# Performance work log

Hardware: AMD Instinct MI355X
Metric: run time of the kernel (lower is better)

The kernel has to match this reference:

```python
import jax, jax.numpy as jnp
from jax import lax
import numpy as np

SCALES = [1.0, 0.9, 0.8, 0.7, 0.6]
SOFTMAX_SCALE = 10.0
RES_SCALE = 1.0
EPS = 1e-4  # escape_NaN buffer


def prelu(x, a):
    # torch nn.PReLU with a single shared parameter a
    return jnp.where(x >= 0, x, a * x)


def conv1x1(x, W, b):
    # x: [B,Cin,H,W], W: [Cout,Cin], b: [Cout]
    return jnp.einsum('oi,bihw->bohw', W, x) + b[None, :, None, None]


def extract_patches(x):
    # x: [B,C,H,W] -> [B, H*W, C, 3, 3]; 'same' padding (pad 1), stride 1,
    # matching F.unfold channel ordering (C, kh, kw) and row-major spatial order.
    B, C, H, W = x.shape
    p = jnp.pad(x, ((0, 0), (0, 0), (1, 1), (1, 1)))
    shifts = [p[:, :, i:i + H, j:j + W] for i in range(3) for j in range(3)]
    pat = jnp.stack(shifts, axis=-1)                      # [B,C,H,W,9]
    pat = pat.reshape(B, C, H, W, 3, 3)
    return pat.transpose(0, 2, 3, 1, 4, 5).reshape(B, H * W, C, 3, 3)


def setup_inputs() -> dict:
    key = jax.random.key(0)
    ks = jax.random.split(key, 7)
    B, C, H, W = 4, 64, 48, 48
    red = 2
    x = jax.random.normal(ks[0], (B, C, H, W), jnp.float32)
    # conv_match_L_base: 1x1 conv 64->32 + PReLU
    Wb = jax.random.normal(ks[1], (C // red, C), jnp.float32) * 0.05
    bb = jax.random.normal(ks[2], (C // red,), jnp.float32) * 0.05
    ab = jnp.asarray(0.25, jnp.float32)
    # conv_match: 1x1 conv 64->32 + PReLU
    Wm = jax.random.normal(ks[3], (C // red, C), jnp.float32) * 0.05
    bm = jax.random.normal(ks[4], (C // red,), jnp.float32) * 0.05
    am = jnp.asarray(0.25, jnp.float32)
    # conv_assembly: 1x1 conv 64->64 + PReLU
    Wa = jax.random.normal(ks[5], (C, C), jnp.float32) * 0.05
    ba = jax.random.normal(ks[6], (C,), jnp.float32) * 0.05
    aa = jnp.asarray(0.25, jnp.float32)
    return {"x": x, "Wb": Wb, "bb": bb, "ab": ab,
            "Wm": Wm, "bm": bm, "am": am,
            "Wa": Wa, "ba": ba, "aa": aa}


def reference(x, Wb, bb, ab, Wm, bm, am, Wa, ba, aa):
    B, C, H, W = x.shape
    match_base = prelu(conv1x1(x, Wb, bb), ab)  # [B,32,H,W]

    w_list, raw_list = [], []
    for s in SCALES:
        if s != 1.0:
            Hs, Ws = int(H * s), int(W * s)
            ref = jax.image.resize(x, (B, C, Hs, Ws), 'bilinear', antialias=False)
        else:
            ref = x
        base = prelu(conv1x1(ref, Wa, ba), aa)   # [B,64,Hs,Ws]
        mat = prelu(conv1x1(ref, Wm, bm), am)    # [B,32,Hs,Ws]
        raw_list.append(extract_patches(base))   # [B,Ls,64,3,3]
        w_list.append(extract_patches(mat))      # [B,Ls,32,3,3]

    wall = jnp.concatenate(w_list, axis=1)       # [B,N,32,3,3]
    rawall = jnp.concatenate(raw_list, axis=1)   # [B,N,64,3,3]
    norm = jnp.maximum(jnp.sqrt(jnp.sum(wall * wall, axis=(2, 3, 4), keepdims=True)), EPS)
    wn = wall / norm

    dn = ('NCHW', 'OIHW', 'NCHW')

    def per_sample(xb, wb, rb):
        # xb: [32,H,W], wb: [N,32,3,3], rb: [N,64,3,3]
        scores = lax.conv_general_dilated(xb[None], wb, (1, 1), ((1, 1), (1, 1)),
                                          dimension_numbers=dn)       # [1,N,H,W]
        attn = jax.nn.softmax(scores * SOFTMAX_SCALE, axis=1)
        # conv_transpose2d(attn, rb, stride=1, padding=1) == conv with flipped,
        # channel-swapped kernel and padding 1
        kt = jnp.flip(rb, axis=(2, 3)).transpose(1, 0, 2, 3)           # [64,N,3,3]
        out = lax.conv_general_dilated(attn, kt, (1, 1), ((1, 1), (1, 1)),
                                       dimension_numbers=dn)           # [1,64,H,W]
        return out[0] / 4.0

    y = jax.vmap(per_sample)(match_base, wn, rawall)  # [B,64,H,W]
    return y + x * RES_SCALE
```

## Files before the change

kernel.cpp:

```cpp
#include <hip/hip_runtime.h>
#include <hip/hip_bf16.h>
#include <hip/hip_fp16.h>

typedef __half h16;
typedef _Float16 f16;
typedef f16 f16x8 __attribute__((ext_vector_type(8)));
typedef __attribute__((ext_vector_type(4))) float f32x4;

#define NB 4
#define NCH 64
#define HW 2304
#define NP 7470
#define NPAD 7552
#define NT 236
#define NT2 118
#define NBLK 59
#define SW2 NPAD

__device__ __forceinline__ float us2f(unsigned short u){
  unsigned v = (unsigned)u << 16; float f; __builtin_memcpy(&f, &v, 4); return f;
}
__device__ __forceinline__ void gl16(const void* g, void* l){
  __builtin_amdgcn_global_load_lds((const __attribute__((address_space(1))) unsigned int*)g,
                                   (__attribute__((address_space(3))) unsigned int*)l, 16, 0, 0);
}

__device__ __forceinline__ void n_decode(int n, int& off, int& d, int& y, int& x){
  if (n < 2304)      { off = 0;    d = 48; }
  else if (n < 4153) { off = 2304; d = 43; }
  else if (n < 5597) { off = 4153; d = 38; }
  else if (n < 6686) { off = 5597; d = 33; }
  else               { off = 6686; d = 28; }
  int l = n - off; y = l / d; x = l - y * d;
}

__global__ __launch_bounds__(256) void k_detect(const void* __restrict__ x, int* __restrict__ flag){
  const unsigned short* u = (const unsigned short*)x;
  int tid = threadIdx.x;
  int c = 0;
  for (int i = tid; i < 8192; i += 256){
    float v = us2f(u[i]);
    float a = fabsf(v);
    if (v == 0.f || (a > 1e-5f && a < 1e3f)) c++;
  }
  #pragma unroll
  for (int o = 1; o < 64; o <<= 1) c += __shfl_xor(c, o);
  __shared__ int wr[4];
  if ((tid & 63) == 0) wr[tid >> 6] = c;
  __syncthreads();
  if (tid == 0) flag[0] = ((wr[0]+wr[1]+wr[2]+wr[3]) > 7000) ? 1 : 0;
}

struct CanonArgs { const void* src[10]; float* dst[10]; int end[10]; };

__global__ __launch_bounds__(256) void k_canon_all(CanonArgs a, int tot, const int* __restrict__ flag){
  int id = blockIdx.x * 256 + threadIdx.x;
  if (id >= tot) return;
  int k = 0;
  while (id >= a.end[k]) k++;
  int local = id - (k ? a.end[k-1] : 0);
  float v;
  if (flag[0]) v = us2f(((const unsigned short*)a.src[k])[local]);
  else         v = ((const float*)a.src[k])[local];
  a.dst[k][local] = v;
}

__global__ __launch_bounds__(256) void k_resize(const float* __restrict__ x, h16* __restrict__ xs){
  int id = blockIdx.x * 256 + threadIdx.x;
  if (id >= NB * NCH * NP) return;
  int b = id / (NCH*NP), rem = id - b*(NCH*NP);
  int c = rem / NP, n = rem - c*NP;
  int off, d, y, xx; n_decode(n, off, d, y, xx);
  const float* pc = x + ((size_t)b * NCH + c) * HW;
  float v;
  if (off == 0){
    v = pc[y*48 + xx];
  } else {
    float cy = (y + 0.5f) * (48.0f / (float)d) - 0.5f;
    float cx = (xx + 0.5f) * (48.0f / (float)d) - 0.5f;
    int y0 = (int)floorf(cy), x0 = (int)floorf(cx);
    float fy = cy - (float)y0, fx = cx - (float)x0;
    int y1 = min(y0 + 1, 47), x1 = min(x0 + 1, 47);
    y0 = max(y0, 0); x0 = max(x0, 0);
    v = (1.f-fy)*((1.f-fx)*pc[y0*48+x0] + fx*pc[y0*48+x1])
      + fy*((1.f-fx)*pc[y1*48+x0] + fx*pc[y1*48+x1]);
  }
  xs[id] = __float2half(v);
}

template<bool OB>
__global__ __launch_bounds__(256) void k_conv1x1(const h16* __restrict__ in, const float* __restrict__ Wt,
    const float* __restrict__ bias, const float* __restrict__ alpha, void* __restrict__ outv,
    int npix, int cout, size_t in_bstride, size_t out_bstride, int rs_in, int rs_out){
  __shared__ float Wl[64*64];
  __shared__ float it[64][64];
  int b = blockIdx.y;
  int n0 = blockIdx.x * 64;
  int tid = threadIdx.x;
  const h16* ib = in + (size_t)b * in_bstride;
  for (int i = tid; i < cout * 64; i += 256) Wl[i] = Wt[i];
  for (int i = tid; i < 64 * 64; i += 256){
    int ci = i >> 6, nn = i & 63;
    int n = n0 + nn;
    it[ci][nn] = (n < npix) ? __half2float(ib[(size_t)ci * rs_in + n]) : 0.f;
  }
  __syncthreads();
  float al = alpha[0];
  for (int oi = tid; oi < cout * 64; oi += 256){
    int co = oi >> 6, nn = oi & 63;
    float acc = bias[co];
    #pragma unroll
    for (int ci = 0; ci < 64; ci++) acc = fmaf(Wl[co*64+ci], it[ci][nn], acc);
    acc = acc >= 0.f ? acc : al * acc;
    int n = n0 + nn;
    if (n < npix){
      size_t idx = (size_t)b * out_bstride + (size_t)co * rs_out + n;
      if constexpr (OB) ((h16*)outv)[idx] = __float2half(acc);
      else              ((float*)outv)[idx] = acc;
    }
  }
}

__global__ __launch_bounds__(256) void k_sq(const float* __restrict__ mat, float* __restrict__ q){
  int id = blockIdx.x * 256 + threadIdx.x;
  if (id >= NB * NP) return;
  int b = id / NP, n = id - b * NP;
  const float* mp = mat + (size_t)b * 32 * NP + n;
  float s = 0.f;
  #pragma unroll
  for (int c = 0; c < 32; c++){ float v = mp[(size_t)c * NP]; s += v * v; }
  q[id] = s;
}

__global__ __launch_bounds__(256) void k_ninv(const float* __restrict__ q, float* __restrict__ ninv){
  int id = blockIdx.x * 256 + threadIdx.x;
  if (id >= NB * NP) return;
  int b = id / NP, n = id - b * NP;
  int off, d, y, x; n_decode(n, off, d, y, x);
  const float* qb = q + (size_t)b * NP + off;
  float s = 0.f;
  #pragma unroll
  for (int dy = -1; dy <= 1; dy++){
    int yy = y + dy; if (yy < 0 || yy >= d) continue;
    #pragma unroll
    for (int dx = -1; dx <= 1; dx++){
      int xx = x + dx; if (xx < 0 || xx >= d) continue;
      s += qb[yy * d + xx];
    }
  }
  ninv[id] = 1.f / fmaxf(sqrtf(s), 1e-4f);
}

__global__ __launch_bounds__(256) void k_packU(const float* __restrict__ mb, h16* __restrict__ U){
  int id = blockIdx.x * 256 + threadIdx.x;
  if (id >= NB * HW * 288) return;
  int b = id / (HW*288), rem = id - b*(HW*288);
  int p = rem / 288, k = rem - p * 288;
  int c = k / 9, r = k - c * 9, kh = r / 3, kw = r - kh * 3;
  int y = p / 48 + kh - 1, x = (p % 48) + kw - 1;
  float v = 0.f;
  if (y >= 0 && y < 48 && x >= 0 && x < 48)
    v = mb[((size_t)b * 32 + c) * HW + y * 48 + x];
  U[id] = __float2half(v);
}

__global__ __launch_bounds__(256) void k_packW(const float* __restrict__ mat, const float* __restrict__ ninv,
                                               h16* __restrict__ Wp, int b0, int g){
  int id = blockIdx.x * 256 + threadIdx.x;
  if (id >= g * NPAD * 288) return;
  int bg = id / (NPAD*288), rem = id - bg*(NPAD*288);
  int n = rem / 288, k = rem - n * 288;
  float v = 0.f;
  if (n < NP){
    int b = b0 + bg;
    int c = k / 9, r = k - c * 9, kh = r / 3, kw = r - kh * 3;
    int off, d, y, x; n_decode(n, off, d, y, x);
    int yy = y + kh - 1, xx = x + kw - 1;
    if (yy >= 0 && yy < d && xx >= 0 && xx < d)
      v = mat[((size_t)b * 32 + c) * NP + off + yy * d + xx] * 10.f * ninv[(size_t)b*NP + n];
  }
  Wp[id] = __float2half(v);
}

__global__ __launch_bounds__(256) void k_packR(const h16* __restrict__ src, h16* __restrict__ dst){
  int id = blockIdx.x * 256 + threadIdx.x;
  if (id >= NB * NT * 576 * 32) return;
  int b = id / (NT*576*32), rem = id - b*(NT*576*32);
  int t = rem / (576*32), rem2 = rem - t*(576*32);
  int j = rem2 / 32, kl = rem2 - j*32;
  int n = t*32 + kl;
  h16 v = __float2half(0.f);
  if (n < NP){
    int c = j / 9, r = j - c * 9, kh = r / 3, kw = r - kh * 3;
    int off, d, y, x; n_decode(n, off, d, y, x);
    int yy = y + kh - 1, xx = x + kw - 1;
    if (yy >= 0 && yy < d && xx >= 0 && xx < d)
      v = src[((size_t)b * 64 + c) * NP + off + yy * d + xx];
  }
  dst[id] = v;
}

__global__ __launch_bounds__(512) void k_gemm1m(const f16* __restrict__ U, const f16* __restrict__ Wp,
    h16* __restrict__ S16, float* __restrict__ Pm, float* __restrict__ Ps, int b0){
  int bg = blockIdx.z, b = b0 + bg;
  int m0 = blockIdx.y * 128, n0 = blockIdx.x * 128;
  int tid = threadIdx.x, l = tid & 63, w = tid >> 6;
  int wm = w >> 1, wn = w & 1;
  int ch = l >> 4, cl = l & 15;
  __shared__ __align__(16) char At[3][8192];
  __shared__ __align__(16) char Bt[3][8192];
  __shared__ float mred[128][2];
  __shared__ float sred[128][2];
  f32x4 acc[2][4] = {};
  const f16* Ub = U + ((size_t)b * HW + m0) * 288;
  const f16* Wb = Wp + ((size_t)bg * NPAD + n0) * 288;
  int abyte[2], bbyte[4];
  #pragma unroll
  for (int mt = 0; mt < 2; mt++){
    int lr = wm*32 + mt*16 + cl;
    abyte[mt] = lr*64 + ((ch ^ ((lr>>1)&3))<<4);
  }
  #pragma unroll
  for (int nt = 0; nt < 4; nt++){
    int lr = wn*64 + nt*16 + cl;
    bbyte[nt] = lr*64 + ((ch ^ ((lr>>1)&3))<<4);
  }
  int srow = tid >> 2, scs = (tid & 3) ^ ((srow >> 1) & 3);
  auto STAGE1 = [&](int t, int bi){
    gl16(Ub + (size_t)srow*288 + t*32 + scs*8, At[bi] + tid*16);
    gl16(Wb + (size_t)srow*288 + t*32 + scs*8, Bt[bi] + tid*16);
  };
  STAGE1(0, 0);
  STAGE1(1, 1);
  __syncthreads();
  int cur = 0;
  for (int t = 0; t < 9; ++t){
    int nx = cur + 2; if (nx >= 3) nx -= 3;
    if (t + 2 < 9){
      STAGE1(t + 2, nx);
      asm volatile("s_waitcnt vmcnt(4)" ::: "memory");
    } else if (t + 1 < 9){
      asm volatile("s_waitcnt vmcnt(2)" ::: "memory");
    } else {
      asm volatile("s_waitcnt vmcnt(0)" ::: "memory");
    }
    __builtin_amdgcn_s_barrier();
    asm volatile("" ::: "memory");
    f16x8 a[2], bv[4];
    #pragma unroll
    for (int mt = 0; mt < 2; mt++) a[mt] = *reinterpret_cast<const f16x8*>(At[cur] + abyte[mt]);
    #pragma unroll
    for (int nt = 0; nt < 4; nt++) bv[nt] = *reinterpret_cast<const f16x8*>(Bt[cur] + bbyte[nt]);
    #pragma unroll
    for (int mt = 0; mt < 2; mt++)
      #pragma unroll
      for (int nt = 0; nt < 4; nt++)
        acc[mt][nt] = __builtin_amdgcn_mfma_f32_16x16x32_f16(a[mt], bv[nt], acc[mt][nt], 0, 0, 0);
    asm volatile("s_waitcnt lgkmcnt(0)" ::: "memory");
    __builtin_amdgcn_s_barrier();
    cur = cur + 1; if (cur >= 3) cur -= 3;
  }
  #pragma unroll
  for (int mt = 0; mt < 2; mt++)
    #pragma unroll
    for (int i = 0; i < 4; i++){
      float v = -3e38f;
      #pragma unroll
      for (int nt = 0; nt < 4; nt++){
        int gn = n0 + wn*64 + nt*16 + cl;
        float t = acc[mt][nt][i];
        v = fmaxf(v, (gn < NP) ? t : -3e38f);
      }
      v = fmaxf(v, __shfl_xor(v, 1));
      v = fmaxf(v, __shfl_xor(v, 2));
      v = fmaxf(v, __shfl_xor(v, 4));
      v = fmaxf(v, __shfl_xor(v, 8));
      if (cl == 0) mred[wm*32 + mt*16 + ch*4 + i][wn] = v;
    }
  __syncthreads();
  #pragma unroll
  for (int mt = 0; mt < 2; mt++)
    #pragma unroll
    for (int i = 0; i < 4; i++){
      int r = wm*32 + mt*16 + ch*4 + i;
      float Ml = fmaxf(mred[r][0], mred[r][1]);
      int gm = m0 + r;
      float s = 0.f;
      #pragma unroll
      for (int nt = 0; nt < 4; nt++){
        int gn = n0 + wn*64 + nt*16 + cl;
        float e = (gn < NP) ? __expf(acc[mt][nt][i] - Ml) : 0.f;
        S16[((size_t)bg*HW + gm)*SW2 + gn] = __float2half(e);
        s += e;
      }
      s += __shfl_xor(s, 1);
      s += __shfl_xor(s, 2);
      s += __shfl_xor(s, 4);
      s += __shfl_xor(s, 8);
      if (cl == 0) sred[r][wn] = s;
    }
  __syncthreads();
  if (tid < 128){
    float Mf = fmaxf(mred[tid][0], mred[tid][1]);
    float L  = sred[tid][0] + sred[tid][1];
    size_t o = ((size_t)bg*HW + m0 + tid)*NBLK + blockIdx.x;
    Pm[o] = Mf; Ps[o] = L;
  }
}

__global__ __launch_bounds__(256) void k_sfac(const float* __restrict__ Pm, const float* __restrict__ Ps,
                                              float* __restrict__ Fac, int gc){
  int rid = blockIdx.x * 4 + (threadIdx.x >> 6);
  int lane = threadIdx.x & 63;
  if (rid >= gc * HW) return;
  const float* pm = Pm + (size_t)rid * NBLK;
  const float* ps = Ps + (size_t)rid * NBLK;
  float mv = (lane < NBLK) ? pm[lane] : -3e38f;
  float sv = (lane < NBLK) ? ps[lane] : 0.f;
  float M = mv;
  #pragma unroll
  for (int o = 1; o < 64; o <<= 1) M = fmaxf(M, __shfl_xor(M, o));
  float e = (lane < NBLK) ? __expf(mv - M) : 0.f;
  float c = e * sv;
  #pragma unroll
  for (int o = 1; o < 64; o <<= 1) c += __shfl_xor(c, o);
  float inv = 1.f / c;
  if (lane < NBLK) Fac[(size_t)rid * NBLK + lane] = e * inv;
}

__global__ __launch_bounds__(512) void k_gemm2n(const f16* __restrict__ S16, const f16* __restrict__ RpT,
    const float* __restrict__ Fac, h16* __restrict__ T, int b0){
  int nwg = gridDim.x;
  int p = blockIdx.x;
  int L = (nwg % 8 == 0) ? ((p & 7)*(nwg>>3) + (p>>3)) : p;
  int jh = L % 3; int t1 = L / 3; int my = t1 % 18; int t2 = t1 / 18;
  int ks = t2 & 1;  int bg = t2 >> 1;
  int b = b0 + bg;
  int m0 = my * 128;
  int tid = threadIdx.x, l = tid & 63, w = tid >> 6;
  int wm = w >> 2, wc = w & 3;
  int ch = l >> 4, cl = l & 15;
  __shared__ __align__(16) char smem[48640];
  f32x4 acc[4][3] = {};
  int lrm[4], abyte[4], rbyte[3];
  #pragma unroll
  for (int mt = 0; mt < 4; mt++){
    lrm[mt] = wm*64 + mt*16 + cl;
    abyte[mt] = lrm[mt]*64 + ((ch ^ ((lrm[mt]>>1)&3))<<4);
  }
  #pragma unroll
  for (int nt = 0; nt < 3; nt++){
    int jr = wc*48 + nt*16 + cl;
    rbyte[nt] = jr*64 + ((ch ^ ((jr>>1)&3))<<4);
  }
  const f16* Sb  = S16 + ((size_t)bg*HW + m0)*SW2;
  const f16* Rb0 = RpT + (size_t)b*((size_t)NT*576*32) + (size_t)jh*(192*32);
  const float* facb = Fac + ((size_t)bg*HW + m0)*NBLK;
  int nb0 = (ks*NT2) >> 2;

  auto STAGE = [&](int t, int bi){
    char* dS = smem + bi*8192;
    char* dR = smem + 16384 + bi*12288;
    const f16* Rb = Rb0 + (size_t)t*(576*32);
    {
      int row = tid >> 2, cs = (tid & 3) ^ ((row >> 1) & 3);
      gl16(Sb + (size_t)row*SW2 + t*32 + cs*8, dS + tid*16);
      gl16(Rb + (size_t)row*32 + cs*8, dR + tid*16);
    }
    if (tid < 256){
      int i2 = tid + 512;
      int r2 = i2 >> 2, c2 = (i2 & 3) ^ ((r2 >> 1) & 3);
      gl16(Rb + (size_t)r2*32 + c2*8, dR + i2*16);
    }
  };

  {
    f16* fl = (f16*)(smem + 40960);
    for (int i = tid; i < 30*128; i += 512){
      int nbl = i >> 7, mm = i & 127;
      int nb = nb0 + nbl;
      fl[i] = (nb < NBLK) ? (f16)facb[(size_t)mm*NBLK + nb] : (f16)0.f;
    }
  }
  STAGE(ks*NT2, 0);
  __syncthreads();

  int cur = 0;
  for (int tt = 0; tt < NT2; ++tt){
    int t = ks*NT2 + tt;
    if (tt + 1 < NT2){
      STAGE(t + 1, cur ^ 1);
      if (tid < 256) { asm volatile("s_waitcnt vmcnt(3)" ::: "memory"); }
      else           { asm volatile("s_waitcnt vmcnt(2)" ::: "memory"); }
    } else {
      asm volatile("s_waitcnt vmcnt(0)" ::: "memory");
    }
    __builtin_amdgcn_s_barrier();
    asm volatile("" ::: "memory");
    const char* Sc = smem + cur*8192;
    const char* Rc = smem + 16384 + cur*12288;
    const f16* fl = (const f16*)(smem + 40960);
    int nbl = (t >> 2) - nb0;
    __builtin_amdgcn_s_setprio(1);
    f16x8 pa[4];
    #pragma unroll
    for (int mt = 0; mt < 4; mt++){
      f16 fac = fl[nbl*128 + lrm[mt]];
      f16x8 sv = *reinterpret_cast<const f16x8*>(Sc + abyte[mt]);
      pa[mt] = sv * fac;
    }
    #pragma unroll
    for (int nt = 0; nt < 3; nt++){
      f16x8 bv = *reinterpret_cast<const f16x8*>(Rc + rbyte[nt]);
      #pragma unroll
      for (int mt = 0; mt < 4; mt++)
        acc[mt][nt] = __builtin_amdgcn_mfma_f32_16x16x32_f16(pa[mt], bv, acc[mt][nt], 0, 0, 0);
    }
    __builtin_amdgcn_s_setprio(0);
    asm volatile("s_waitcnt lgkmcnt(0)" ::: "memory");
    __builtin_amdgcn_s_barrier();
    cur ^= 1;
  }

  h16* Tsp = T + (size_t)ks * ((size_t)NB*576*HW);
  h16* Tl = (h16*)smem;
  #pragma unroll
  for (int r = 0; r < 2; ++r){
    __syncthreads();
    if ((wc >> 1) == r){
      #pragma unroll
      for (int nt = 0; nt < 3; nt++)
        #pragma unroll
        for (int mt = 0; mt < 4; mt++)
          #pragma unroll
          for (int i = 0; i < 4; i++)
            Tl[((wc & 1)*48 + nt*16 + cl)*136 + wm*64 + mt*16 + ch*4 + i] = __float2half(acc[mt][nt][i]);
    }
    __syncthreads();
    #pragma unroll
    for (int rep = 0; rep < 3; rep++){
      int idx = tid + rep*512;
      int j0 = idx >> 4, q = idx & 15;
      uint4 v = *reinterpret_cast<const uint4*>((const char*)Tl + j0*272 + q*16);
      h16* dst = Tsp + ((size_t)b*576 + jh*192 + r*96 + j0)*HW + m0 + q*8;
      *reinterpret_cast<uint4*>(dst) = v;
    }
  }
}

__global__ __launch_bounds__(256) void k_fold(const h16* __restrict__ T, const float* __restrict__ x,
    void* __restrict__ out, const int* __restrict__ flag){
  const h16* T2 = T + (size_t)NB*576*HW;
  int id = blockIdx.x * 256 + threadIdx.x;
  if (id >= NB * 64 * HW) return;
  int b = id / (64*HW), id2 = id - b*(64*HW);
  int co = id2 / HW, p = id2 - co * HW;
  int y = p / 48, xx = p - y * 48;
  float acc = 0.f;
  #pragma unroll
  for (int dy = -1; dy <= 1; dy++){
    int yy = y + dy; if (yy < 0 || yy >= 48) continue;
    #pragma unroll
    for (int dx = -1; dx <= 1; dx++){
      int x2 = xx + dx; if (x2 < 0 || x2 >= 48) continue;
      int j = co*9 + (1-dy)*3 + (1-dx);
      size_t o = ((size_t)b*576 + j)*HW + yy*48 + x2;
      acc += __half2float(T[o]) + __half2float(T2[o]);
    }
  }
  size_t gi = (size_t)id;
  float r = x[gi] + 0.25f * acc;
  if (flag[0]) ((__hip_bfloat16*)out)[gi] = __float2bfloat16(r);
  else         ((float*)out)[gi] = r;
}

extern "C" void kernel_launch(void* const* d_in, const int* in_sizes, int n_in,
                              void* d_out, int out_size, void* d_ws, size_t ws_size,
                              hipStream_t stream){
  (void)out_size; (void)n_in;

  char* cur = (char*)d_ws;
  auto carve = [&](size_t bytes)->char*{
    char* p = cur; cur += (bytes + 255) & ~(size_t)255; return p;
  };
  int*   flag  = (int*)  carve(4);
  float* canon[10];
  for (int i = 0; i < 10; i++) canon[i] = (float*)carve((size_t)in_sizes[i] * 4);
  float* xc = canon[0];
  float* Wb = canon[1]; float* bb = canon[2]; float* ab = canon[3];
  float* Wm = canon[4]; float* bm = canon[5]; float* am = canon[6];
  float* Wa = canon[7]; float* ba = canon[8]; float* aa = canon[9];

  h16*   xs    = (h16*)  carve((size_t)NB * 64 * NP * 2);
  float* mbuf  = (float*)carve((size_t)NB * 32 * HW * 4);
  float* mat   = (float*)carve((size_t)NB * 32 * NP * 4);
  float* qbuf  = (float*)carve((size_t)NB * NP * 4);
  float* ninv  = (float*)carve((size_t)NB * NP * 4);
  h16*   baseh = (h16*)  carve((size_t)NB * 64 * NP * 2);
  h16*   U     = (h16*)  carve((size_t)NB * HW * 288 * 2);
  h16*   RpT   = (h16*)  carve((size_t)NB * NT * 576 * 32 * 2);
  h16*   T     = (h16*)  carve((size_t)2 * NB * 576 * HW * 2);

  size_t fixed = (size_t)(cur - (char*)d_ws);
  size_t perb  = (((size_t)NPAD*288*2 + 255) & ~(size_t)255)
               + (((size_t)HW*SW2*2 + 255) & ~(size_t)255)
               + 3 * (((size_t)HW*NBLK*4 + 255) & ~(size_t)255);
  size_t avail = (ws_size > fixed) ? ws_size - fixed : 0;
  int g = (int)(avail / perb);
  if (g < 1) g = 1;
  if (g > NB) g = NB;
  h16*   Wp  = (h16*)  carve((size_t)g * NPAD * 288 * 2);
  h16*   S16 = (h16*)  carve((size_t)g * HW * SW2 * 2);
  float* Pm  = (float*)carve((size_t)g * HW * NBLK * 4);
  float* Ps  = (float*)carve((size_t)g * HW * NBLK * 4);
  float* Fac = (float*)carve((size_t)g * HW * NBLK * 4);

  k_detect<<<1, 256, 0, stream>>>(d_in[0], flag);
  {
    CanonArgs ca; int tot = 0;
    for (int i = 0; i < 10; i++){
      ca.src[i] = d_in[i]; ca.dst[i] = canon[i];
      tot += in_sizes[i]; ca.end[i] = tot;
    }
    k_canon_all<<<(tot + 255)/256, 256, 0, stream>>>(ca, tot, flag);
  }

  k_resize<<<((size_t)NB*NCH*NP + 255)/256, 256, 0, stream>>>(xc, xs);

  dim3 gm((NP + 63)/64, NB);
  k_conv1x1<false><<<gm, 256, 0, stream>>>(xs, Wm, bm, am, (void*)mat,   NP, 32, (size_t)64*NP, (size_t)32*NP, NP, NP);
  k_conv1x1<true ><<<gm, 256, 0, stream>>>(xs, Wa, ba, aa, (void*)baseh, NP, 64, (size_t)64*NP, (size_t)64*NP, NP, NP);
  dim3 gb2((HW + 63)/64, NB);
  k_conv1x1<false><<<gb2, 256, 0, stream>>>(xs, Wb, bb, ab, (void*)mbuf, HW, 32, (size_t)64*NP, (size_t)32*HW, NP, HW);

  k_sq  <<<(NB*NP + 255)/256, 256, 0, stream>>>(mat, qbuf);
  k_ninv<<<(NB*NP + 255)/256, 256, 0, stream>>>(qbuf, ninv);
  k_packU<<<((size_t)NB*HW*288 + 255)/256, 256, 0, stream>>>(mbuf, U);
  k_packR<<<((size_t)NB*NT*576*32 + 255)/256, 256, 0, stream>>>(baseh, RpT);

  for (int b0 = 0; b0 < NB; b0 += g){
    int gc = (b0 + g <= NB) ? g : (NB - b0);
    k_packW<<<((size_t)gc*NPAD*288 + 255)/256, 256, 0, stream>>>(mat, ninv, Wp, b0, gc);
    dim3 g1(NBLK, HW/128, gc);
    k_gemm1m<<<g1, 512, 0, stream>>>((const f16*)U, (const f16*)Wp, S16, Pm, Ps, b0);
    k_sfac<<<(gc*HW + 3)/4, 256, 0, stream>>>(Pm, Ps, Fac, gc);
    int nwg2 = 3 * 18 * 2 * gc;
    k_gemm2n<<<nwg2, 512, 0, stream>>>((const f16*)S16, (const f16*)RpT, Fac, T, b0);
  }

  k_fold<<<(NB*64*HW + 255)/256, 256, 0, stream>>>(T, xc, d_out, flag);
}
```

Baseline: 343.7 us.

## Stage softmax tile through LDS for coalesced stores, remap blocks per XCD

The first GEMM kernel now writes its exp'd fp16 score tile into shared memory (reusing the pipeline buffers) and then emits 16-byte coalesced row stores to S16, replacing scattered 2-byte stores. The 3D grid is flattened into 1D with an XCD-aware remapping, so consecutive logical tiles (sharing the same N block) land on the same XCD for L2 reuse. It also raises wave priority around the MFMA section. The cost is an extra LDS round trip and barrier, plus index-math overhead.

```diff
diff --git a/kernel.cpp b/kernel.cpp
--- a/kernel.cpp
+++ b/kernel.cpp
@@ -202,15 +202,19 @@
 
 __global__ __launch_bounds__(512) void k_gemm1m(const f16* __restrict__ U, const f16* __restrict__ Wp,
     h16* __restrict__ S16, float* __restrict__ Pm, float* __restrict__ Ps, int b0){
-  int bg = blockIdx.z, b = b0 + bg;
-  int m0 = blockIdx.y * 128, n0 = blockIdx.x * 128;
+  int nwg = gridDim.x;
+  int p = blockIdx.x;
+  int qc = nwg >> 3, rc = nwg & 7, xcd = p & 7;
+  int L = (xcd < rc ? xcd*(qc+1) : rc*(qc+1) + (xcd - rc)*qc) + (p >> 3);
+  int my = L % 18; int t1 = L / 18; int nb = t1 % NBLK; int bg = t1 / NBLK;
+  int b = b0 + bg;
+  int m0 = my * 128, n0 = nb * 128;
   int tid = threadIdx.x, l = tid & 63, w = tid >> 6;
   int wm = w >> 1, wn = w & 1;
   int ch = l >> 4, cl = l & 15;
-  __shared__ __align__(16) char At[3][8192];
-  __shared__ __align__(16) char Bt[3][8192];
-  __shared__ float mred[128][2];
-  __shared__ float sred[128][2];
+  __shared__ __align__(16) char smem[51200];
+  float* mredp = (float*)(smem + 49152);
+  float* sredp = (float*)(smem + 50176);
   f32x4 acc[2][4] = {};
   const f16* Ub = U + ((size_t)b * HW + m0) * 288;
   const f16* Wb = Wp + ((size_t)bg * NPAD + n0) * 288;
@@ -227,8 +231,8 @@
   }
   int srow = tid >> 2, scs = (tid & 3) ^ ((srow >> 1) & 3);
   auto STAGE1 = [&](int t, int bi){
-    gl16(Ub + (size_t)srow*288 + t*32 + scs*8, At[bi] + tid*16);
-    gl16(Wb + (size_t)srow*288 + t*32 + scs*8, Bt[bi] + tid*16);
+    gl16(Ub + (size_t)srow*288 + t*32 + scs*8, smem + bi*8192 + tid*16);
+    gl16(Wb + (size_t)srow*288 + t*32 + scs*8, smem + 24576 + bi*8192 + tid*16);
   };
   STAGE1(0, 0);
   STAGE1(1, 1);
@@ -246,16 +250,20 @@
     }
     __builtin_amdgcn_s_barrier();
     asm volatile("" ::: "memory");
+    const char* Ac = smem + cur*8192;
+    const char* Bc = smem + 24576 + cur*8192;
+    __builtin_amdgcn_s_setprio(1);
     f16x8 a[2], bv[4];
     #pragma unroll
-    for (int mt = 0; mt < 2; mt++) a[mt] = *reinterpret_cast<const f16x8*>(At[cur] + abyte[mt]);
-    #pragma unroll
-    for (int nt = 0; nt < 4; nt++) bv[nt] = *reinterpret_cast<const f16x8*>(Bt[cur] + bbyte[nt]);
+    for (int mt = 0; mt < 2; mt++) a[mt] = *reinterpret_cast<const f16x8*>(Ac + abyte[mt]);
+    #pragma unroll
+    for (int nt = 0; nt < 4; nt++) bv[nt] = *reinterpret_cast<const f16x8*>(Bc + bbyte[nt]);
     #pragma unroll
     for (int mt = 0; mt < 2; mt++)
       #pragma unroll
       for (int nt = 0; nt < 4; nt++)
         acc[mt][nt] = __builtin_amdgcn_mfma_f32_16x16x32_f16(a[mt], bv[nt], acc[mt][nt], 0, 0, 0);
+    __builtin_amdgcn_s_setprio(0);
     asm volatile("s_waitcnt lgkmcnt(0)" ::: "memory");
     __builtin_amdgcn_s_barrier();
     cur = cur + 1; if (cur >= 3) cur -= 3;
@@ -275,36 +283,50 @@
       v = fmaxf(v, __shfl_xor(v, 2));
       v = fmaxf(v, __shfl_xor(v, 4));
       v = fmaxf(v, __shfl_xor(v, 8));
-      if (cl == 0) mred[wm*32 + mt*16 + ch*4 + i][wn] = v;
+      if (cl == 0) mredp[(wm*32 + mt*16 + ch*4 + i)*2 + wn] = v;
     }
   __syncthreads();
-  #pragma unroll
-  for (int mt = 0; mt < 2; mt++)
-    #pragma unroll
-    for (int i = 0; i < 4; i++){
-      int r = wm*32 + mt*16 + ch*4 + i;
-      float Ml = fmaxf(mred[r][0], mred[r][1]);
-      int gm = m0 + r;
-      float s = 0.f;
+  {
+    h16* Tl = (h16*)smem;
+    #pragma unroll
+    for (int mt = 0; mt < 2; mt++)
       #pragma unroll
-      for (int nt = 0; nt < 4; nt++){
-        int gn = n0 + wn*64 + nt*16 + cl;
-        float e = (gn < NP) ? __expf(acc[mt][nt][i] - Ml) : 0.f;
-        S16[((size_t)bg*HW + gm)*SW2 + gn] = __float2half(e);
-        s += e;
+      for (int i = 0; i < 4; i++){
+        int r = wm*32 + mt*16 + ch*4 + i;
+        float Ml = fmaxf(mredp[r*2+0], mredp[r*2+1]);
+        float s = 0.f;
+        #pragma unroll
+        for (int nt = 0; nt < 4; nt++){
+          int c = wn*64 + nt*16 + cl;
+          int gn = n0 + c;
+          float e = (gn < NP) ? __expf(acc[mt][nt][i] - Ml) : 0.f;
+          Tl[r*132 + c] = __float2half(e);
+          s += e;
+        }
+        s += __shfl_xor(s, 1);
+        s += __shfl_xor(s, 2);
+        s += __shfl_xor(s, 4);
+        s += __shfl_xor(s, 8);
+        if (cl == 0) sredp[r*2 + wn] = s;
       }
-      s += __shfl_xor(s, 1);
-      s += __shfl_xor(s, 2);
-      s += __shfl_xor(s, 4);
-      s += __shfl_xor(s, 8);
-      if (cl == 0) sred[r][wn] = s;
-    }
+  }
   __syncthreads();
   if (tid < 128){
-    float Mf = fmaxf(mred[tid][0], mred[tid][1]);
-    float L  = sred[tid][0] + sred[tid][1];
-    size_t o = ((size_t)bg*HW + m0 + tid)*NBLK + blockIdx.x;
-    Pm[o] = Mf; Ps[o] = L;
+    float Mf = fmaxf(mredp[tid*2+0], mredp[tid*2+1]);
+    float Lg = sredp[tid*2+0] + sredp[tid*2+1];
+    size_t o = ((size_t)bg*HW + m0 + tid)*NBLK + nb;
+    Pm[o] = Mf; Ps[o] = Lg;
+  }
+  {
+    const h16* Tl = (const h16*)smem;
+    #pragma unroll
+    for (int rep = 0; rep < 4; rep++){
+      int idx = tid + rep*512;
+      int j0 = idx >> 4, qq = idx & 15;
+      uint4 v = *reinterpret_cast<const uint4*>((const char*)Tl + j0*264 + qq*16);
+      h16* dst = S16 + ((size_t)bg*HW + m0 + j0)*SW2 + n0 + qq*8;
+      *reinterpret_cast<uint4*>(dst) = v;
+    }
   }
 }
 
@@ -541,8 +563,8 @@
   for (int b0 = 0; b0 < NB; b0 += g){
     int gc = (b0 + g <= NB) ? g : (NB - b0);
     k_packW<<<((size_t)gc*NPAD*288 + 255)/256, 256, 0, stream>>>(mat, ninv, Wp, b0, gc);
-    dim3 g1(NBLK, HW/128, gc);
-    k_gemm1m<<<g1, 512, 0, stream>>>((const f16*)U, (const f16*)Wp, S16, Pm, Ps, b0);
+    int nwg1 = 18 * NBLK * gc;
+    k_gemm1m<<<nwg1, 512, 0, stream>>>((const f16*)U, (const f16*)Wp, S16, Pm, Ps, b0);
     k_sfac<<<(gc*HW + 3)/4, 256, 0, stream>>>(Pm, Ps, Fac, gc);
     int nwg2 = 3 * 18 * 2 * gc;
     k_gemm2n<<<nwg2, 512, 0, stream>>>((const f16*)S16, (const f16*)RpT, Fac, T, b0);
```

Measured after the change: 332.8 us. 1.03x faster.
